# Kernel tuning notes

Measured on AMD Instinct MI355X. Metric: run time of the kernel, lower is better.

Reference implementation:

```python
import jax, jax.numpy as jnp
import numpy as np

N_STOCKS = 65536
HIDDEN = 512
N_INDUSTRIES = 128
NEG_SLOPE = 0.01  # nn.LeakyReLU default


def setup_inputs() -> dict:
    key = jax.random.key(0)
    k1, k2, k3 = jax.random.split(key, 3)
    e_s = jax.random.normal(k1, (N_STOCKS, HIDDEN), dtype=jnp.float32)
    # one industry per stock -> exactly N_STOCKS ones in the incidence matrix
    ind = jax.random.randint(k2, (N_STOCKS,), 0, N_INDUSTRIES)
    industry_matrix = jax.nn.one_hot(ind, N_INDUSTRIES, dtype=jnp.int32)
    # HypergraphConv params: lin (no bias) + output bias
    weight = jax.random.normal(k3, (HIDDEN, HIDDEN), dtype=jnp.float32) / np.sqrt(HIDDEN)
    bias = jnp.zeros((HIDDEN,), dtype=jnp.float32)
    return {"e_s": e_s, "industry_matrix": industry_matrix, "weight": weight, "bias": bias}


def reference(e_s, industry_matrix, weight, bias):
    N, H = e_s.shape
    E = industry_matrix.shape[1]
    # torch.where(industry_matrix == 1): static size N (one-hot rows)
    stock_idx, ind_idx = jnp.nonzero(industry_matrix == 1, size=N)
    x = e_s @ weight  # lin projection
    ones = jnp.ones((N,), dtype=e_s.dtype)
    # node degree D (hyperedge_weight defaults to 1) and edge degree B
    D = jax.ops.segment_sum(ones, stock_idx, num_segments=N)
    Dinv = jnp.where(D > 0, 1.0 / D, 0.0)
    B = jax.ops.segment_sum(ones, ind_idx, num_segments=E)
    Binv = jnp.where(B > 0, 1.0 / B, 0.0)
    # node -> hyperedge: B^{-1} H^T X Theta
    edge_feat = jax.ops.segment_sum(x[stock_idx], ind_idx, num_segments=E) * Binv[:, None]
    # hyperedge -> node: D^{-1} H (edge_feat)
    out = jax.ops.segment_sum(edge_feat[ind_idx], stock_idx, num_segments=N) * Dinv[:, None]
    out = out + bias
    # LeakyReLU
    return jnp.where(out >= 0, out, NEG_SLOPE * out)
```

## Files before the change

### kernel.cpp

```cpp
#include <hip/hip_runtime.h>

#define NS 65536
#define HID 512
#define NE 128
#define NEG 0.01f

typedef int   vi4 __attribute__((ext_vector_type(4)));
typedef float vf4 __attribute__((ext_vector_type(4)));

__global__ __launch_bounds__(1024) void k_find(const int* __restrict__ im,
                                               int* __restrict__ ind) {
    __shared__ int lind[256];
    const int b = blockIdx.x, t = threadIdx.x;
    const vi4* p = reinterpret_cast<const vi4*>(im) + (size_t)b * 8192;
#pragma unroll
    for (int j = t; j < 8192; j += 1024) {
        vi4 v = __builtin_nontemporal_load(p + j);
        int s = j >> 5;
        int c = (j & 31) << 2;
        if (v[0] == 1) lind[s] = c;
        if (v[1] == 1) lind[s] = c + 1;
        if (v[2] == 1) lind[s] = c + 2;
        if (v[3] == 1) lind[s] = c + 3;
    }
    __syncthreads();
    if (t < 256) ind[b * 256 + t] = lind[t];
}

__global__ __launch_bounds__(1024) void k_agg(const float* __restrict__ e_s,
                                              const int* __restrict__ ind,
                                              float* __restrict__ partial,
                                              int* __restrict__ counts) {
    __shared__ int rows[1024];
    __shared__ vf4 red[1024];
    __shared__ int cntL;
    const int e = blockIdx.x >> 2;
    const int q = blockIdx.x & 3;
    const int t = threadIdx.x;
    if (t == 0) cntL = 0;
    __syncthreads();
    const int base = q * (NS / 4);
#pragma unroll
    for (int k = 0; k < (NS / 4) / 1024; ++k) {
        int idx = base + k * 1024 + t;
        if (ind[idx] == e) {
            int p = atomicAdd(&cntL, 1);
            if (p < 1024) rows[p] = idx;
        }
    }
    __syncthreads();
    const int cnt = (cntL < 1024) ? cntL : 1024;
    const int g = t >> 7;
    const int l = t & 127;
    vf4 acc = {0.f, 0.f, 0.f, 0.f};
#pragma unroll 4
    for (int i = g; i < cnt; i += 8) {
        int row = rows[i];
        vf4 v = __builtin_nontemporal_load(
            reinterpret_cast<const vf4*>(e_s + (size_t)row * HID) + l);
        acc += v;
    }
    red[t] = acc;
    __syncthreads();
    if (g == 0) {
        vf4 a = red[l];
#pragma unroll
        for (int p = 1; p < 8; ++p) a += red[l + p * 128];
        reinterpret_cast<vf4*>(partial + ((size_t)(q * NE + e)) * HID)[l] = a;
    }
    if (t == 0) counts[q * NE + e] = cnt;
}

__global__ __launch_bounds__(1024) void k_gemm(const float* __restrict__ partial,
                                               const float* __restrict__ W,
                                               const float* __restrict__ bias,
                                               const int* __restrict__ counts,
                                               float* __restrict__ efrow) {
    __shared__ float aL[HID];
    __shared__ float redf[1024];
    const int e = blockIdx.x;
    const int t = threadIdx.x;
    if (t < HID) {
        float s = 0.f;
#pragma unroll
        for (int q = 0; q < 4; ++q) s += partial[((size_t)(q * NE + e)) * HID + t];
        aL[t] = s;
    }
    __syncthreads();
    const int j  = t & (HID - 1);
    const int hh = t >> 9;
    const int k0 = hh * 256;
    float acc = 0.f;
#pragma unroll 8
    for (int k = k0; k < k0 + 256; ++k)
        acc += aL[k] * W[k * HID + j];
    redf[t] = acc;
    __syncthreads();
    if (t < HID) {
        int tot = counts[e] + counts[NE + e] + counts[2 * NE + e] + counts[3 * NE + e];
        float binv = (tot > 0) ? 1.0f / (float)tot : 0.0f;
        float v = (redf[t] + redf[t + HID]) * binv + bias[t];
        efrow[(size_t)e * HID + t] = (v >= 0.0f) ? v : NEG * v;
    }
}

__global__ __launch_bounds__(1024) void k_out(const float* __restrict__ efrow,
                                              const int* __restrict__ ind,
                                              float* __restrict__ out) {
    __shared__ int lindL[256];
    const int b = blockIdx.x, t = threadIdx.x;
    if (t < 256) lindL[t] = ind[b * 256 + t];
    __syncthreads();
    const int g = t >> 7;
    const int l = t & 127;
    vf4* outp = reinterpret_cast<vf4*>(out) + (size_t)b * 256 * 128;
#pragma unroll 4
    for (int ls = g; ls < 256; ls += 8) {
        int e = lindL[ls];
        vf4 v = reinterpret_cast<const vf4*>(efrow + (size_t)e * HID)[l];
        __builtin_nontemporal_store(v, outp + ls * 128 + l);
    }
}

extern "C" void kernel_launch(void* const* d_in, const int* in_sizes, int n_in,
                              void* d_out, int out_size, void* d_ws, size_t ws_size,
                              hipStream_t stream) {
    const float* e_s  = (const float*)d_in[0];
    const int*   im   = (const int*)d_in[1];
    const float* W    = (const float*)d_in[2];
    const float* bias = (const float*)d_in[3];
    float* out = (float*)d_out;

    char* ws = (char*)d_ws;
    int*   ind     = (int*)(ws + 0);
    float* partial = (float*)(ws + 262144);
    float* efrow   = (float*)(ws + 262144);
    int*   counts  = (int*)(ws + 1310720);

    k_find<<<256, 1024, 0, stream>>>(im, ind);
    k_agg <<<NE * 4, 1024, 0, stream>>>(e_s, ind, partial, counts);
    k_gemm<<<NE, 1024, 0, stream>>>(partial, W, bias, counts, efrow);
    k_out <<<256, 1024, 0, stream>>>(efrow, ind, out);
}
```

Baseline: 76.95 us.

## Replace per-industry gather with row-chunk shared-atomic scatter accumulation

Industry indices are now stored as bytes, and k_find also emits a per-block industry histogram that replaces the old count scan. Each k_accum block takes a contiguous 512-row chunk and a 128-column slice of e_s. It scatters the rows into a shared per-industry accumulator with LDS atomics, then writes the whole accumulator out as a partial. This removes the repeated full-index scans per industry and the indirect row gathers. In exchange it writes and rereads a large partial buffer (512 x 128 x 128 floats), and k_gemm must reduce 128 partials per industry with strided loads. It also relies on shared-memory float atomics.

Result: slower. 238.3 us (+209.7%).

```diff
diff --git a/kernel.cpp b/kernel.cpp
--- a/kernel.cpp
+++ b/kernel.cpp
@@ -7,11 +7,15 @@
 
 typedef int   vi4 __attribute__((ext_vector_type(4)));
 typedef float vf4 __attribute__((ext_vector_type(4)));
+typedef unsigned char uchar;
 
 __global__ __launch_bounds__(1024) void k_find(const int* __restrict__ im,
-                                               int* __restrict__ ind) {
+                                               uchar* __restrict__ ind8,
+                                               int* __restrict__ bhist) {
     __shared__ int lind[256];
+    __shared__ int lhist[NE];
     const int b = blockIdx.x, t = threadIdx.x;
+    if (t < NE) lhist[t] = 0;
     const vi4* p = reinterpret_cast<const vi4*>(im) + (size_t)b * 8192;
 #pragma unroll
     for (int j = t; j < 8192; j += 1024) {
@@ -24,80 +28,75 @@
         if (v[3] == 1) lind[s] = c + 3;
     }
     __syncthreads();
-    if (t < 256) ind[b * 256 + t] = lind[t];
+    if (t < 256) {
+        int e = lind[t];
+        ind8[b * 256 + t] = (uchar)e;
+        atomicAdd(&lhist[e], 1);
+    }
+    __syncthreads();
+    if (t < NE) bhist[b * NE + t] = lhist[t];
 }
 
-__global__ __launch_bounds__(1024) void k_agg(const float* __restrict__ e_s,
-                                              const int* __restrict__ ind,
-                                              float* __restrict__ partial,
-                                              int* __restrict__ counts) {
-    __shared__ int rows[1024];
-    __shared__ vf4 red[1024];
-    __shared__ int cntL;
-    const int e = blockIdx.x >> 2;
-    const int q = blockIdx.x & 3;
+__global__ __launch_bounds__(1024) void k_accum(const float* __restrict__ e_s,
+                                                const uchar* __restrict__ ind8,
+                                                float* __restrict__ partial) {
+    __shared__ float acc[NE * 128];
+    __shared__ int indL[512];
+    const int c = blockIdx.x >> 2;
+    const int j = blockIdx.x & 3;
     const int t = threadIdx.x;
-    if (t == 0) cntL = 0;
+    for (int k = t; k < NE * 128; k += 1024) acc[k] = 0.f;
+    if (t < 512) indL[t] = ind8[c * 512 + t];
     __syncthreads();
-    const int base = q * (NS / 4);
-#pragma unroll
-    for (int k = 0; k < (NS / 4) / 1024; ++k) {
-        int idx = base + k * 1024 + t;
-        if (ind[idx] == e) {
-            int p = atomicAdd(&cntL, 1);
-            if (p < 1024) rows[p] = idx;
-        }
+    const int g = t >> 6;
+    const int l = t & 63;
+    const float* bp = e_s + ((size_t)c * 512) * HID + j * 128;
+#pragma unroll 4
+    for (int r = g; r < 512; r += 16) {
+        int e = indL[r];
+        float v0 = __builtin_nontemporal_load(bp + (size_t)r * HID + l);
+        float v1 = __builtin_nontemporal_load(bp + (size_t)r * HID + l + 64);
+        atomicAdd(&acc[e * 128 + l], v0);
+        atomicAdd(&acc[e * 128 + l + 64], v1);
     }
     __syncthreads();
-    const int cnt = (cntL < 1024) ? cntL : 1024;
-    const int g = t >> 7;
-    const int l = t & 127;
-    vf4 acc = {0.f, 0.f, 0.f, 0.f};
-#pragma unroll 4
-    for (int i = g; i < cnt; i += 8) {
-        int row = rows[i];
-        vf4 v = __builtin_nontemporal_load(
-            reinterpret_cast<const vf4*>(e_s + (size_t)row * HID) + l);
-        acc += v;
-    }
-    red[t] = acc;
-    __syncthreads();
-    if (g == 0) {
-        vf4 a = red[l];
-#pragma unroll
-        for (int p = 1; p < 8; ++p) a += red[l + p * 128];
-        reinterpret_cast<vf4*>(partial + ((size_t)(q * NE + e)) * HID)[l] = a;
-    }
-    if (t == 0) counts[q * NE + e] = cnt;
+    vf4* dst = reinterpret_cast<vf4*>(partial + (size_t)blockIdx.x * (NE * 128));
+    const vf4* src = reinterpret_cast<const vf4*>(acc);
+    for (int k = t; k < (NE * 128) / 4; k += 1024) dst[k] = src[k];
 }
 
 __global__ __launch_bounds__(1024) void k_gemm(const float* __restrict__ partial,
+                                               const int* __restrict__ bhist,
                                                const float* __restrict__ W,
                                                const float* __restrict__ bias,
-                                               const int* __restrict__ counts,
                                                float* __restrict__ efrow) {
     __shared__ float aL[HID];
     __shared__ float redf[1024];
-    const int e = blockIdx.x;
-    const int t = threadIdx.x;
-    if (t < HID) {
+    __shared__ int cntS;
+    const int e = blockIdx.x, t = threadIdx.x;
+    if (t == 0) cntS = 0;
+    __syncthreads();
+    if (t < 256) atomicAdd(&cntS, bhist[t * NE + e]);
+    if (t < 512) {
+        const int jj = t >> 7, x = t & 127;
         float s = 0.f;
-#pragma unroll
-        for (int q = 0; q < 4; ++q) s += partial[((size_t)(q * NE + e)) * HID + t];
-        aL[t] = s;
+#pragma unroll 8
+        for (int cc = 0; cc < 128; ++cc)
+            s += partial[((size_t)(cc * 4 + jj)) * (NE * 128) + e * 128 + x];
+        aL[jj * 128 + x] = s;
     }
     __syncthreads();
-    const int j  = t & (HID - 1);
+    const int jcol = t & (HID - 1);
     const int hh = t >> 9;
     const int k0 = hh * 256;
     float acc = 0.f;
 #pragma unroll 8
     for (int k = k0; k < k0 + 256; ++k)
-        acc += aL[k] * W[k * HID + j];
+        acc += aL[k] * W[k * HID + jcol];
     redf[t] = acc;
     __syncthreads();
     if (t < HID) {
-        int tot = counts[e] + counts[NE + e] + counts[2 * NE + e] + counts[3 * NE + e];
+        int tot = cntS;
         float binv = (tot > 0) ? 1.0f / (float)tot : 0.0f;
         float v = (redf[t] + redf[t + HID]) * binv + bias[t];
         efrow[(size_t)e * HID + t] = (v >= 0.0f) ? v : NEG * v;
@@ -105,11 +104,11 @@
 }
 
 __global__ __launch_bounds__(1024) void k_out(const float* __restrict__ efrow,
-                                              const int* __restrict__ ind,
+                                              const uchar* __restrict__ ind8,
                                               float* __restrict__ out) {
     __shared__ int lindL[256];
     const int b = blockIdx.x, t = threadIdx.x;
-    if (t < 256) lindL[t] = ind[b * 256 + t];
+    if (t < 256) lindL[t] = ind8[b * 256 + t];
     __syncthreads();
     const int g = t >> 7;
     const int l = t & 127;
@@ -132,13 +131,13 @@
     float* out = (float*)d_out;
 
     char* ws = (char*)d_ws;
-    int*   ind     = (int*)(ws + 0);
-    float* partial = (float*)(ws + 262144);
-    float* efrow   = (float*)(ws + 262144);
-    int*   counts  = (int*)(ws + 1310720);
+    uchar* ind8    = (uchar*)(ws + 0);
+    int*   bhist   = (int*)(ws + 65536);
+    float* efrow   = (float*)(ws + 196608);
+    float* partial = (float*)(ws + 524288);
 
-    k_find<<<256, 1024, 0, stream>>>(im, ind);
-    k_agg <<<NE * 4, 1024, 0, stream>>>(e_s, ind, partial, counts);
-    k_gemm<<<NE, 1024, 0, stream>>>(partial, W, bias, counts, efrow);
-    k_out <<<256, 1024, 0, stream>>>(efrow, ind, out);
+    k_find <<<256, 1024, 0, stream>>>(im, ind8, bhist);
+    k_accum<<<512, 1024, 0, stream>>>(e_s, ind8, partial);
+    k_gemm <<<NE, 1024, 0, stream>>>(partial, bhist, W, bias, efrow);
+    k_out  <<<256, 1024, 0, stream>>>(efrow, ind8, out);
 }
```
